# Optimization experiments

Measured on AMD Instinct MI355X. Metric: run time of the kernel, lower is better.

## Reference

```python
import jax, jax.numpy as jnp
import numpy as np

EMBED = 1024
HEADS = 16
DK = EMBED // HEADS
DFF = 4 * EMBED
EPS = 1e-5


def layer_norm(x, g, b):
    mu = jnp.mean(x, axis=-1, keepdims=True)
    var = jnp.var(x, axis=-1, keepdims=True)
    return (x - mu) * jax.lax.rsqrt(var + EPS) * g + b


def setup_inputs() -> dict:
    key = jax.random.key(0)
    ks = jax.random.split(key, 12)
    s = lambda d: 1.0 / np.sqrt(d)
    return {
        "x": jax.random.normal(ks[0], (4, 1024, EMBED), dtype=jnp.float32),
        "norm_g": jnp.ones((EMBED,), jnp.float32),
        "norm_b": jnp.zeros((EMBED,), jnp.float32),
        "w_qkv": jax.random.normal(ks[1], (EMBED, 3 * EMBED), jnp.float32) * s(EMBED),
        "b_qkv": jnp.zeros((3 * EMBED,), jnp.float32),
        "w_proj": jax.random.normal(ks[2], (EMBED, EMBED), jnp.float32) * s(EMBED),
        "b_proj": jnp.zeros((EMBED,), jnp.float32),
        "w_fc1": jax.random.normal(ks[3], (EMBED, DFF), jnp.float32) * s(EMBED),
        "b_fc1": jnp.zeros((DFF,), jnp.float32),
        "w_fc2": jax.random.normal(ks[4], (DFF, EMBED), jnp.float32) * s(DFF),
        "b_fc2": jnp.zeros((EMBED,), jnp.float32),
    }


def reference(x, norm_g, norm_b, w_qkv, b_qkv, w_proj, b_proj, w_fc1, b_fc1, w_fc2, b_fc2):
    B, N, C = x.shape
    # --- attention branch (pre-norm, shared norm params) ---
    h = layer_norm(x, norm_g, norm_b)
    qkv = (h @ w_qkv + b_qkv).reshape(B, N, 3, HEADS, DK)
    q, k, v = jnp.moveaxis(qkv, 2, 0)  # each [B, N, H, dk]
    # NOTE: source divides by dk**(-0.5), i.e. multiplies scores by sqrt(dk)
    scores = jnp.einsum('bnhd,bmhd->bhnm', q, k) * (DK ** 0.5)
    attn = jax.nn.softmax(scores, axis=-1)
    ctx = jnp.einsum('bhnm,bmhd->bnhd', attn, v).reshape(B, N, C)
    x = x + (ctx @ w_proj + b_proj)
    # --- MLP branch ---
    h = layer_norm(x, norm_g, norm_b)
    h = jax.nn.gelu(h @ w_fc1 + b_fc1, approximate=False)
    x = x + (h @ w_fc2 + b_fc2)
    return x
```

## Files before the change

### kernel.cpp

```cpp
#include <hip/hip_runtime.h>
#include <hip/hip_bf16.h>

typedef __attribute__((ext_vector_type(8))) short short8;
typedef __attribute__((ext_vector_type(8))) _Float16 half8;
typedef __attribute__((ext_vector_type(4))) float f32x4;

__device__ __forceinline__ unsigned short f2h(float f) {
    _Float16 h = (_Float16)f;
    return *reinterpret_cast<unsigned short*>(&h);
}
__device__ __forceinline__ float h2f(unsigned short u) {
    _Float16 h = *reinterpret_cast<_Float16*>(&u);
    return (float)h;
}

__device__ __forceinline__ void gld_lds16(const unsigned short* g, unsigned short* l) {
    __builtin_amdgcn_global_load_lds(
        (const __attribute__((address_space(1))) unsigned int*)g,
        (__attribute__((address_space(3))) unsigned int*)l, 16, 0, 0);
}

__global__ __launch_bounds__(256)
void transpose_all(const float* __restrict__ W0, const float* __restrict__ W1,
                   const float* __restrict__ W2, const float* __restrict__ W3,
                   unsigned short* __restrict__ o0, unsigned short* __restrict__ o1,
                   unsigned short* __restrict__ o2, unsigned short* __restrict__ o3) {
    __shared__ float tile[32][33];
    const int bid = blockIdx.x;
    const float* W; unsigned short* out; int K, N, loc;
    if (bid < 3072)      { W = W0; out = o0; K = 1024; N = 3072; loc = bid; }
    else if (bid < 4096) { W = W1; out = o1; K = 1024; N = 1024; loc = bid - 3072; }
    else if (bid < 8192) { W = W2; out = o2; K = 1024; N = 4096; loc = bid - 4096; }
    else                 { W = W3; out = o3; K = 4096; N = 1024; loc = bid - 8192; }
    const int nx = N >> 5;
    const int n0 = (loc % nx) << 5, k0 = (loc / nx) << 5;
    const int tid = threadIdx.x;
    const int r = tid >> 3, c4 = (tid & 7) << 2;
    float4 v = *reinterpret_cast<const float4*>(W + (size_t)(k0 + r) * N + n0 + c4);
    tile[r][c4 + 0] = v.x; tile[r][c4 + 1] = v.y;
    tile[r][c4 + 2] = v.z; tile[r][c4 + 3] = v.w;
    __syncthreads();
    const int n = n0 + r;
    ushort4 o;
    o.x = f2h(tile[c4 + 0][r]); o.y = f2h(tile[c4 + 1][r]);
    o.z = f2h(tile[c4 + 2][r]); o.w = f2h(tile[c4 + 3][r]);
    *reinterpret_cast<ushort4*>(out + (size_t)n * K + k0 + c4) = o;
}

__global__ __launch_bounds__(256)
void ln_kernel(const float* __restrict__ x, const float* __restrict__ gw,
               const float* __restrict__ bw, unsigned short* __restrict__ out) {
    const int row = blockIdx.x, tid = threadIdx.x;
    const float* xr = x + (size_t)row * 1024;
    float4 v = *reinterpret_cast<const float4*>(xr + tid * 4);
    float s = v.x + v.y + v.z + v.w;
    float sq = v.x * v.x + v.y * v.y + v.z * v.z + v.w * v.w;
    #pragma unroll
    for (int off = 1; off < 64; off <<= 1) {
        s  += __shfl_xor(s, off);
        sq += __shfl_xor(sq, off);
    }
    __shared__ float ps[4], pq[4];
    const int wave = tid >> 6;
    if ((tid & 63) == 0) { ps[wave] = s; pq[wave] = sq; }
    __syncthreads();
    s  = ps[0] + ps[1] + ps[2] + ps[3];
    sq = pq[0] + pq[1] + pq[2] + pq[3];
    const float mu = s * (1.0f / 1024.0f);
    const float var = sq * (1.0f / 1024.0f) - mu * mu;
    const float rs = rsqrtf(var + 1e-5f);
    float4 gv = *reinterpret_cast<const float4*>(gw + tid * 4);
    float4 bv = *reinterpret_cast<const float4*>(bw + tid * 4);
    ushort4 o;
    o.x = f2h((v.x - mu) * rs * gv.x + bv.x);
    o.y = f2h((v.y - mu) * rs * gv.y + bv.y);
    o.z = f2h((v.z - mu) * rs * gv.z + bv.z);
    o.w = f2h((v.w - mu) * rs * gv.w + bv.w);
    *reinterpret_cast<ushort4*>(out + (size_t)row * 1024 + tid * 4) = o;
}

template<int EPI, int NZ>
__global__ __launch_bounds__(512, 4)
void gemm_mid(const unsigned short* __restrict__ A, const unsigned short* __restrict__ Bt,
              const float* __restrict__ bias, void* Cout,
              int M, int N, int K, int lda, int ldb, int ldc) {
    __shared__ unsigned short As[2][128 * 32];
    __shared__ unsigned short Bs[2][256 * 32];
    const int tid = threadIdx.x;
    const int wave = tid >> 6, lane = tid & 63;
    const int nx = N >> 8;
    int bm, bn, z;
    if (NZ == 1) {
        const int nwg = gridDim.x;
        const int swz = (blockIdx.x & 7) * (nwg >> 3) + (blockIdx.x >> 3);
        bm = (swz / nx) << 7; bn = (swz % nx) << 8; z = 0;
    } else {
        int bid = blockIdx.x;
        const int xcd = bid & 7; int rest = bid >> 3;
        bn = (rest % nx) << 8; rest /= nx;
        z = rest % NZ; rest /= NZ;
        bm = (rest * 8 + xcd) << 7;
    }
    const size_t koff = (size_t)z * K;
    const int wm = wave >> 2, wn = wave & 3;
    const int fr = lane & 15, g8 = (lane >> 4) << 3, fq = (lane >> 4) << 2;
    const int jq = g8 >> 3;
    const int sx2 = (fr >> 1) & 3;

    const int srow = lane >> 2;
    const int scol = ((lane & 3) ^ ((lane >> 3) & 3)) << 3;
    const unsigned short* gA  = A + (size_t)(bm + wave * 16 + srow) * lda + scol + koff;
    const unsigned short* gB0 = Bt + (size_t)(bn + wave * 32 + srow) * ldb + scol + koff;
    const unsigned short* gB1 = gB0 + (size_t)16 * ldb;
    const int lbA = wave * 512;
    const int lbB = wave * 1024;

    f32x4 acc[4][4];
    #pragma unroll
    for (int m = 0; m < 4; ++m)
        #pragma unroll
        for (int n_ = 0; n_ < 4; ++n_)
            #pragma unroll
            for (int r_ = 0; r_ < 4; ++r_) acc[m][n_][r_] = 0.0f;

    auto stage = [&](int buf, int k0) {
        gld_lds16(gA + k0, &As[buf][lbA]);
        gld_lds16(gB0 + k0, &Bs[buf][lbB]);
        gld_lds16(gB1 + k0, &Bs[buf][lbB + 512]);
    };
    auto compute = [&](int buf) {
        half8 af[4], bfv[4];
        #pragma unroll
        for (int m = 0; m < 4; ++m)
            af[m] = *reinterpret_cast<const half8*>(
                &As[buf][(wm * 64 + m * 16 + fr) * 32 + ((jq ^ sx2) << 3)]);
        #pragma unroll
        for (int n_ = 0; n_ < 4; ++n_)
            bfv[n_] = *reinterpret_cast<const half8*>(
                &Bs[buf][(wn * 64 + n_ * 16 + fr) * 32 + ((jq ^ sx2) << 3)]);
        #pragma unroll
        for (int m = 0; m < 4; ++m)
            #pragma unroll
            for (int n_ = 0; n_ < 4; ++n_)
                acc[m][n_] = __builtin_amdgcn_mfma_f32_16x16x32_f16(af[m], bfv[n_], acc[m][n_], 0, 0, 0);
    };

    const int nt = K >> 5;
    stage(0, 0);
    __syncthreads();
    int k0 = 32;
    for (int t = 0; t < nt - 2; t += 2) {
        stage(1, k0);
        compute(0);
        __syncthreads();
        stage(0, k0 + 32);
        compute(1);
        __syncthreads();
        k0 += 64;
    }
    stage(1, k0);
    compute(0);
    __syncthreads();
    compute(1);

    if (EPI == 4) {
        unsigned short* P = reinterpret_cast<unsigned short*>(Cout) +
                            (size_t)z * (size_t)M * ldc;
        #pragma unroll
        for (int n_ = 0; n_ < 4; ++n_) {
            const int col = bn + wn * 64 + n_ * 16 + fr;
            #pragma unroll
            for (int m = 0; m < 4; ++m)
                #pragma unroll
                for (int r_ = 0; r_ < 4; ++r_) {
                    const int row = bm + wm * 64 + m * 16 + fq + r_;
                    P[(size_t)row * ldc + col] = f2h(acc[m][n_][r_]);
                }
        }
        return;
    }

    unsigned short* o16 = reinterpret_cast<unsigned short*>(Cout);
    #pragma unroll
    for (int n_ = 0; n_ < 4; ++n_) {
        const int col = bn + wn * 64 + n_ * 16 + fr;
        const float bc = bias[col];
        #pragma unroll
        for (int m = 0; m < 4; ++m) {
            #pragma unroll
            for (int r_ = 0; r_ < 4; ++r_) {
                const int row = bm + wm * 64 + m * 16 + fq + r_;
                const size_t idx = (size_t)row * ldc + col;
                float v = acc[m][n_][r_] + bc;
                if (EPI == 0) {
                    o16[idx] = f2h(v);
                } else {
                    float ge = 0.5f * v * (1.0f + erff(v * 0.70710678118654752f));
                    o16[idx] = f2h(ge);
                }
            }
        }
    }
}

template<int EPI, int BM, int REMAP>
__global__ __launch_bounds__(256)
void gemm_bt(const unsigned short* __restrict__ A, const unsigned short* __restrict__ Bt,
             const float* __restrict__ bias, const float* resid,
             void* Cout, int M, int N, int K, int lda, int ldb, int ldc) {
    constexpr int MF = BM / 32;
    __shared__ unsigned short As[2][BM * 32];
    __shared__ unsigned short Bs[2][128 * 32];
    const int tid = threadIdx.x;
    const int wave = tid >> 6, lane = tid & 63;
    int bm, bn;
    if (REMAP) {
        const int nxr = N >> 7;
        int bid = blockIdx.x;
        const int xcd = bid & 7; int rest = bid >> 3;
        bn = (rest % nxr) << 7; rest /= nxr;
        bm = (rest * 8 + xcd) * BM;
    } else {
        bm = blockIdx.y * BM; bn = blockIdx.x << 7;
    }
    const int wr = (wave >> 1) * (BM / 2), wc = (wave & 1) << 6;
    const int fr = lane & 15, g8 = (lane >> 4) << 3, fq = (lane >> 4) << 2;
    const int jq = g8 >> 3, sx2 = (fr >> 1) & 3;

    const int srowA = (BM == 128) ? ((wave << 5) + (lane >> 2)) : ((wave << 4) + (lane >> 2));
    const int srowB = (wave << 5) + (lane >> 2);
    const int scol = (((lane & 3) ^ ((lane >> 3) & 3))) << 3;
    const unsigned short* gA0 = A + (size_t)(bm + srowA) * lda + scol;
    const unsigned short* gA1 = gA0 + (size_t)16 * lda;
    const unsigned short* gB0 = Bt + (size_t)(bn + srowB) * ldb + scol;
    const unsigned short* gB1 = gB0 + (size_t)16 * ldb;

    f32x4 acc[MF][4];
    #pragma unroll
    for (int m = 0; m < MF; ++m)
        #pragma unroll
        for (int n = 0; n < 4; ++n)
            #pragma unroll
            for (int r = 0; r < 4; ++r) acc[m][n][r] = 0.0f;

    auto stage = [&](int buf, int k0) {
        unsigned short* lA = &As[buf][(BM == 128) ? (wave << 10) : (wave << 9)];
        unsigned short* lB = &Bs[buf][wave << 10];
        gld_lds16(gA0 + k0, lA);
        if constexpr (BM == 128) gld_lds16(gA1 + k0, lA + 512);
        gld_lds16(gB0 + k0, lB);
        gld_lds16(gB1 + k0, lB + 512);
    };
    auto compute = [&](int buf) {
        half8 af[MF], bfv[4];
        #pragma unroll
        for (int m = 0; m < MF; ++m)
            af[m] = *reinterpret_cast<const half8*>(
                &As[buf][(wr + m * 16 + fr) * 32 + ((jq ^ sx2) << 3)]);
        #pragma unroll
        for (int n = 0; n < 4; ++n)
            bfv[n] = *reinterpret_cast<const half8*>(
                &Bs[buf][(wc + n * 16 + fr) * 32 + ((jq ^ sx2) << 3)]);
        #pragma unroll
        for (int m = 0; m < MF; ++m)
            #pragma unroll
            for (int n = 0; n < 4; ++n)
                acc[m][n] = __builtin_amdgcn_mfma_f32_16x16x32_f16(af[m], bfv[n], acc[m][n], 0, 0, 0);
    };

    const int nt = K >> 5;
    stage(0, 0);
    __syncthreads();
    int k0 = 32;
    for (int t = 0; t < nt - 2; t += 2) {
        stage(1, k0);
        compute(0);
        __syncthreads();
        stage(0, k0 + 32);
        compute(1);
        __syncthreads();
        k0 += 64;
    }
    stage(1, k0);
    compute(0);
    __syncthreads();
    compute(1);

    #pragma unroll
    for (int n = 0; n < 4; ++n) {
        const int col = bn + wc + n * 16 + fr;
        const float bc = bias[col];
        #pragma unroll
        for (int m = 0; m < MF; ++m) {
            #pragma unroll
            for (int r = 0; r < 4; ++r) {
                const int row = bm + wr + m * 16 + fq + r;
                const size_t idx = (size_t)row * ldc + col;
                float v = acc[m][n][r] + bc;
                reinterpret_cast<float*>(Cout)[idx] = v + resid[idx];
            }
        }
    }
}

template<int Z>
__global__ __launch_bounds__(256)
void red_h(const unsigned short* __restrict__ p, const float* __restrict__ bias,
           float* out) {
    const size_t MN = (size_t)4096 * 1024;
    const size_t i = ((size_t)blockIdx.x * 256 + threadIdx.x) * 4;
    float4 r  = *reinterpret_cast<const float4*>(out + i);
    float4 bb = *reinterpret_cast<const float4*>(bias + (i & 1023));
    float o0 = r.x + bb.x, o1 = r.y + bb.y, o2 = r.z + bb.z, o3 = r.w + bb.w;
    #pragma unroll
    for (int z = 0; z < Z; ++z) {
        ushort4 a = *reinterpret_cast<const ushort4*>(p + (size_t)z * MN + i);
        o0 += h2f(a.x); o1 += h2f(a.y); o2 += h2f(a.z); o3 += h2f(a.w);
    }
    float4 o; o.x = o0; o.y = o1; o.z = o2; o.w = o3;
    *reinterpret_cast<float4*>(out + i) = o;
}

__global__ __launch_bounds__(256)
void kv_conv(const unsigned short* __restrict__ qkv16, unsigned short* __restrict__ K_g,
             unsigned short* __restrict__ Vt_g) {
    __shared__ unsigned short VtT[64][72];
    const int kc = blockIdx.x;
    const int bh = blockIdx.y;
    const int b = bh >> 4, h = bh & 15;
    const int tid = threadIdx.x;
    const int key = tid >> 2, c16 = (tid & 3) << 4;
    const unsigned short* kp = qkv16 + ((size_t)(b * 1024 + kc * 64 + key)) * 3072 + 1024 + h * 64 + c16;
    alignas(16) unsigned short kbuf[16];
    #pragma unroll
    for (int j = 0; j < 16; j += 8) {
        short8 k8 = *reinterpret_cast<const short8*>(kp + j);
        short8 v8 = *reinterpret_cast<const short8*>(kp + 1024 + j);
        #pragma unroll
        for (int c = 0; c < 8; ++c) {
            kbuf[j + c] = f2h(8.0f * h2f((unsigned short)k8[c]));
            VtT[c16 + j + c][key] = (unsigned short)v8[c];
        }
    }
    const size_t kb = ((size_t)bh * 1024 + kc * 64 + key) * 64 + c16;
    *reinterpret_cast<short8*>(K_g + kb)     = *reinterpret_cast<short8*>(&kbuf[0]);
    *reinterpret_cast<short8*>(K_g + kb + 8) = *reinterpret_cast<short8*>(&kbuf[8]);
    __syncthreads();
    const int d = tid >> 2;
    const size_t vb = ((size_t)bh * 64 + d) * 1024 + (size_t)kc * 64 + c16;
    *reinterpret_cast<short8*>(Vt_g + vb)     = *reinterpret_cast<const short8*>(&VtT[d][c16]);
    *reinterpret_cast<short8*>(Vt_g + vb + 8) = *reinterpret_cast<const short8*>(&VtT[d][c16 + 8]);
}

__global__ __launch_bounds__(256)
void attn_kernel(const unsigned short* __restrict__ qkv16,
                 const unsigned short* __restrict__ K_g,
                 const unsigned short* __restrict__ Vt_g,
                 unsigned short* __restrict__ ctx) {
    __shared__ unsigned short Kh[64][72];
    __shared__ unsigned short Vt[64][72];
    __shared__ unsigned short Plds[4][16][72];
    const int qt = blockIdx.x;
    const int bh = blockIdx.y;
    const int b = bh >> 4, h = bh & 15;
    const int tid = threadIdx.x;
    const int wave = tid >> 6, lane = tid & 63;
    const int fr = lane & 15, g8 = (lane >> 4) << 3, fq = (lane >> 4) << 2;

    const int qrow = qt * 64 + wave * 16 + fr;
    const unsigned short* qp = qkv16 + ((size_t)(b * 1024 + qrow)) * 3072 + h * 64;
    half8 qf[2];
    qf[0] = *reinterpret_cast<const half8*>(qp + g8);
    qf[1] = *reinterpret_cast<const half8*>(qp + 32 + g8);

    float mrun[4], lrun[4];
    f32x4 cacc[4];
    #pragma unroll
    for (int r = 0; r < 4; ++r) { mrun[r] = -3.0e38f; lrun[r] = 0.0f; }
    #pragma unroll
    for (int nd = 0; nd < 4; ++nd)
        #pragma unroll
        for (int r = 0; r < 4; ++r) cacc[nd][r] = 0.0f;

    const int skey = tid >> 2, sc16 = (tid & 3) << 4;
    const unsigned short* kgp = K_g + ((size_t)bh * 1024 + skey) * 64 + sc16;
    const unsigned short* vgp = Vt_g + ((size_t)bh * 64 + skey) * 1024 + sc16;

    short8 ka = *reinterpret_cast<const short8*>(kgp);
    short8 kb = *reinterpret_cast<const short8*>(kgp + 8);
    short8 va = *reinterpret_cast<const short8*>(vgp);
    short8 vb = *reinterpret_cast<const short8*>(vgp + 8);

    for (int kt = 0; kt < 16; ++kt) {
        __syncthreads();
        *reinterpret_cast<short8*>(&Kh[skey][sc16])     = ka;
        *reinterpret_cast<short8*>(&Kh[skey][sc16 + 8]) = kb;
        *reinterpret_cast<short8*>(&Vt[skey][sc16])     = va;
        *reinterpret_cast<short8*>(&Vt[skey][sc16 + 8]) = vb;
        __syncthreads();
        const int ktn = (kt < 15) ? kt + 1 : 15;
        ka = *reinterpret_cast<const short8*>(kgp + (size_t)ktn * 4096);
        kb = *reinterpret_cast<const short8*>(kgp + (size_t)ktn * 4096 + 8);
        va = *reinterpret_cast<const short8*>(vgp + ktn * 64);
        vb = *reinterpret_cast<const short8*>(vgp + ktn * 64 + 8);

        f32x4 S[4];
        #pragma unroll
        for (int n = 0; n < 4; ++n)
            #pragma unroll
            for (int r = 0; r < 4; ++r) S[n][r] = 0.0f;
        #pragma unroll
        for (int s_ = 0; s_ < 2; ++s_)
            #pragma unroll
            for (int n = 0; n < 4; ++n) {
                half8 kh = *reinterpret_cast<const half8*>(&Kh[n * 16 + fr][s_ * 32 + g8]);
                S[n] = __builtin_amdgcn_mfma_f32_16x16x32_f16(qf[s_], kh, S[n], 0, 0, 0);
            }

        float mt[4];
        #pragma unroll
        for (int r = 0; r < 4; ++r)
            mt[r] = fmaxf(fmaxf(S[0][r], S[1][r]), fmaxf(S[2][r], S[3][r]));
        #pragma unroll
        for (int r = 0; r < 4; ++r) {
            mt[r] = fmaxf(mt[r], __shfl_xor(mt[r], 1));
            mt[r] = fmaxf(mt[r], __shfl_xor(mt[r], 2));
            mt[r] = fmaxf(mt[r], __shfl_xor(mt[r], 4));
            mt[r] = fmaxf(mt[r], __shfl_xor(mt[r], 8));
        }
        float P[4][4], rsum[4];
        #pragma unroll
        for (int r = 0; r < 4; ++r) {
            float mnew = fmaxf(mrun[r], mt[r]);
            float sf = __expf(mrun[r] - mnew);
            mrun[r] = mnew;
            rsum[r] = 0.0f;
            #pragma unroll
            for (int n = 0; n < 4; ++n) {
                float p = __expf(S[n][r] - mnew);
                P[n][r] = p;
                rsum[r] += p;
            }
            lrun[r] *= sf;
            #pragma unroll
            for (int nd = 0; nd < 4; ++nd) cacc[nd][r] *= sf;
        }
        #pragma unroll
        for (int r = 0; r < 4; ++r) {
            rsum[r] += __shfl_xor(rsum[r], 1);
            rsum[r] += __shfl_xor(rsum[r], 2);
            rsum[r] += __shfl_xor(rsum[r], 4);
            rsum[r] += __shfl_xor(rsum[r], 8);
            lrun[r] += rsum[r];
        }
        #pragma unroll
        for (int n = 0; n < 4; ++n)
            #pragma unroll
            for (int r = 0; r < 4; ++r)
                Plds[wave][fq + r][n * 16 + fr] = f2h(P[n][r]);
        #pragma unroll
        for (int s_ = 0; s_ < 2; ++s_) {
            half8 pa = *reinterpret_cast<const half8*>(&Plds[wave][fr][s_ * 32 + g8]);
            #pragma unroll
            for (int nd = 0; nd < 4; ++nd) {
                half8 vb8 = *reinterpret_cast<const half8*>(&Vt[nd * 16 + fr][s_ * 32 + g8]);
                cacc[nd] = __builtin_amdgcn_mfma_f32_16x16x32_f16(pa, vb8, cacc[nd], 0, 0, 0);
            }
        }
    }
    #pragma unroll
    for (int r = 0; r < 4; ++r) {
        const float inv = 1.0f / lrun[r];
        const int row = qt * 64 + wave * 16 + fq + r;
        unsigned short* cp = ctx + ((size_t)(b * 1024 + row)) * 1024 + h * 64;
        #pragma unroll
        for (int nd = 0; nd < 4; ++nd)
            cp[nd * 16 + fr] = f2h(cacc[nd][r] * inv);
    }
}

extern "C" void kernel_launch(void* const* d_in, const int* in_sizes, int n_in,
                              void* d_out, int out_size, void* d_ws, size_t ws_size,
                              hipStream_t stream) {
    const float* x      = (const float*)d_in[0];
    const float* norm_g = (const float*)d_in[1];
    const float* norm_b = (const float*)d_in[2];
    const float* w_qkv  = (const float*)d_in[3];
    const float* b_qkv  = (const float*)d_in[4];
    const float* w_proj = (const float*)d_in[5];
    const float* b_proj = (const float*)d_in[6];
    const float* w_fc1  = (const float*)d_in[7];
    const float* b_fc1  = (const float*)d_in[8];
    const float* w_fc2  = (const float*)d_in[9];
    const float* b_fc2  = (const float*)d_in[10];
    float* out = (float*)d_out;
    char* ws = (char*)d_ws;

    size_t off = 0;
    unsigned short* wqkvT  = (unsigned short*)(ws + off); off += (size_t)3072 * 1024 * 2;
    unsigned short* wprojT = (unsigned short*)(ws + off); off += (size_t)1024 * 1024 * 2;
    unsigned short* wfc1T  = (unsigned short*)(ws + off); off += (size_t)4096 * 1024 * 2;
    unsigned short* wfc2T  = (unsigned short*)(ws + off); off += (size_t)1024 * 4096 * 2;
    unsigned short* ctxb   = (unsigned short*)(ws + off); off += (size_t)4096 * 1024 * 2;
    char* G = ws + off;
    unsigned short* h1    = (unsigned short*)G;
    unsigned short* qkv16 = (unsigned short*)(G + (size_t)8388608);
    unsigned short* K_g   = (unsigned short*)G;
    unsigned short* Vt_g  = (unsigned short*)(G + (size_t)33554432);
    unsigned short* fc1o  = (unsigned short*)G;
    unsigned short* h2    = (unsigned short*)(G + (size_t)41943040);
    unsigned short* fc2ph = (unsigned short*)(G + (size_t)33554432);

    transpose_all<<<12288, 256, 0, stream>>>(w_qkv, w_proj, w_fc1, w_fc2,
                                             wqkvT, wprojT, wfc1T, wfc2T);

    ln_kernel<<<4096, 256, 0, stream>>>(x, norm_g, norm_b, h1);
    gemm_mid<0, 1><<<384, 512, 0, stream>>>(h1, wqkvT, b_qkv, qkv16,
                                            4096, 3072, 1024, 1024, 1024, 3072);

    kv_conv<<<dim3(16, 64), 256, 0, stream>>>(qkv16, K_g, Vt_g);

    attn_kernel<<<dim3(16, 64), 256, 0, stream>>>(qkv16, K_g, Vt_g, ctxb);

    gemm_bt<1, 64, 1><<<512, 256, 0, stream>>>(ctxb, wprojT, b_proj, x, out,
                                               4096, 1024, 1024, 1024, 1024, 1024);

    ln_kernel<<<4096, 256, 0, stream>>>(out, norm_g, norm_b, h2);
    gemm_mid<2, 1><<<512, 512, 0, stream>>>(h2, wfc1T, b_fc1, fc1o,
                                            4096, 4096, 1024, 1024, 1024, 4096);

    gemm_mid<4, 4><<<512, 512, 0, stream>>>(fc1o, wfc2T, nullptr, fc2ph,
                                            4096, 1024, 1024, 4096, 4096, 1024);
    red_h<4><<<4096, 256, 0, stream>>>(fc2ph, b_fc2, out);
}
```

Baseline: 262.3 us.

## Use exp2 softmax with lazy rescaling and MFMA row-sum in attention

Result: faster. 249.8 us (-4.8%).

```diff
diff --git a/kernel.cpp b/kernel.cpp
--- a/kernel.cpp
+++ b/kernel.cpp
@@ -332,13 +332,14 @@
     const int key = tid >> 2, c16 = (tid & 3) << 4;
     const unsigned short* kp = qkv16 + ((size_t)(b * 1024 + kc * 64 + key)) * 3072 + 1024 + h * 64 + c16;
     alignas(16) unsigned short kbuf[16];
+    const float KSCALE = 8.0f * 1.44269504088896f;
     #pragma unroll
     for (int j = 0; j < 16; j += 8) {
         short8 k8 = *reinterpret_cast<const short8*>(kp + j);
         short8 v8 = *reinterpret_cast<const short8*>(kp + 1024 + j);
         #pragma unroll
         for (int c = 0; c < 8; ++c) {
-            kbuf[j + c] = f2h(8.0f * h2f((unsigned short)k8[c]));
+            kbuf[j + c] = f2h(KSCALE * h2f((unsigned short)k8[c]));
             VtT[c16 + j + c][key] = (unsigned short)v8[c];
         }
     }
@@ -360,8 +361,8 @@
     __shared__ unsigned short Kh[64][72];
     __shared__ unsigned short Vt[64][72];
     __shared__ unsigned short Plds[4][16][72];
-    const int qt = blockIdx.x;
-    const int bh = blockIdx.y;
+    const int bh = blockIdx.x;
+    const int qt = blockIdx.y;
     const int b = bh >> 4, h = bh & 15;
     const int tid = threadIdx.x;
     const int wave = tid >> 6, lane = tid & 63;
@@ -373,10 +374,14 @@
     qf[0] = *reinterpret_cast<const half8*>(qp + g8);
     qf[1] = *reinterpret_cast<const half8*>(qp + 32 + g8);
 
-    float mrun[4], lrun[4];
-    f32x4 cacc[4];
-    #pragma unroll
-    for (int r = 0; r < 4; ++r) { mrun[r] = -3.0e38f; lrun[r] = 0.0f; }
+    half8 ones;
+    #pragma unroll
+    for (int j = 0; j < 8; ++j) ones[j] = (_Float16)1.0f;
+
+    float mrun[4];
+    f32x4 cacc[4], csum;
+    #pragma unroll
+    for (int r = 0; r < 4; ++r) { mrun[r] = -3.0e38f; csum[r] = 0.0f; }
     #pragma unroll
     for (int nd = 0; nd < 4; ++nd)
         #pragma unroll
@@ -428,36 +433,26 @@
             mt[r] = fmaxf(mt[r], __shfl_xor(mt[r], 4));
             mt[r] = fmaxf(mt[r], __shfl_xor(mt[r], 8));
         }
-        float P[4][4], rsum[4];
-        #pragma unroll
-        for (int r = 0; r < 4; ++r) {
-            float mnew = fmaxf(mrun[r], mt[r]);
-            float sf = __expf(mrun[r] - mnew);
-            mrun[r] = mnew;
-            rsum[r] = 0.0f;
-            #pragma unroll
-            for (int n = 0; n < 4; ++n) {
-                float p = __expf(S[n][r] - mnew);
-                P[n][r] = p;
-                rsum[r] += p;
+        int grow = 0;
+        #pragma unroll
+        for (int r = 0; r < 4; ++r) grow |= (mt[r] > mrun[r] + 8.0f) ? 1 : 0;
+        if (__any(grow)) {
+            #pragma unroll
+            for (int r = 0; r < 4; ++r) {
+                float mnew = fmaxf(mrun[r], mt[r]);
+                float sf = __builtin_amdgcn_exp2f(mrun[r] - mnew);
+                mrun[r] = mnew;
+                csum[r] *= sf;
+                #pragma unroll
+                for (int nd = 0; nd < 4; ++nd) cacc[nd][r] *= sf;
             }
-            lrun[r] *= sf;
-            #pragma unroll
-            for (int nd = 0; nd < 4; ++nd) cacc[nd][r] *= sf;
-        }
-        #pragma unroll
-        for (int r = 0; r < 4; ++r) {
-            rsum[r] += __shfl_xor(rsum[r], 1);
-            rsum[r] += __shfl_xor(rsum[r], 2);
-            rsum[r] += __shfl_xor(rsum[r], 4);
-            rsum[r] += __shfl_xor(rsum[r], 8);
-            lrun[r] += rsum[r];
-        }
-        #pragma unroll
-        for (int n = 0; n < 4; ++n)
-            #pragma unroll
-            for (int r = 0; r < 4; ++r)
-                Plds[wave][fq + r][n * 16 + fr] = f2h(P[n][r]);
+        }
+        #pragma unroll
+        for (int r = 0; r < 4; ++r)
+            #pragma unroll
+            for (int n = 0; n < 4; ++n)
+                Plds[wave][fq + r][n * 16 + fr] =
+                    f2h(__builtin_amdgcn_exp2f(S[n][r] - mrun[r]));
         #pragma unroll
         for (int s_ = 0; s_ < 2; ++s_) {
             half8 pa = *reinterpret_cast<const half8*>(&Plds[wave][fr][s_ * 32 + g8]);
@@ -466,11 +461,12 @@
                 half8 vb8 = *reinterpret_cast<const half8*>(&Vt[nd * 16 + fr][s_ * 32 + g8]);
                 cacc[nd] = __builtin_amdgcn_mfma_f32_16x16x32_f16(pa, vb8, cacc[nd], 0, 0, 0);
             }
+            csum = __builtin_amdgcn_mfma_f32_16x16x32_f16(pa, ones, csum, 0, 0, 0);
         }
     }
     #pragma unroll
     for (int r = 0; r < 4; ++r) {
-        const float inv = 1.0f / lrun[r];
+        const float inv = 1.0f / csum[r];
         const int row = qt * 64 + wave * 16 + fq + r;
         unsigned short* cp = ctx + ((size_t)(b * 1024 + row)) * 1024 + h * 64;
         #pragma unroll
@@ -520,7 +516,7 @@
 
     kv_conv<<<dim3(16, 64), 256, 0, stream>>>(qkv16, K_g, Vt_g);
 
-    attn_kernel<<<dim3(16, 64), 256, 0, stream>>>(qkv16, K_g, Vt_g, ctxb);
+    attn_kernel<<<dim3(64, 16), 256, 0, stream>>>(qkv16, K_g, Vt_g, ctxb);
 
     gemm_bt<1, 64, 1><<<512, 256, 0, stream>>>(ctxb, wprojT, b_proj, x, out,
                                                4096, 1024, 1024, 1024, 1024, 1024);
```
